# Performance work log

Measured on AMD Instinct MI355X. Metric: run time of the kernel, lower is better.

The kernel has to match this reference:

```python
import jax, jax.numpy as jnp
import numpy as np

B, V, T = 8, 16, 64
DIN, H, RH, K, TMP = 6, 256, 64, 2, 256
E = V * (V - 1)
NREL, NPOS = 7, 3  # 2D relative / positional feature counts

_edges = np.ones((V, V)) - np.eye(V)
SEND = jnp.asarray(np.where(_edges)[0])
RECV = jnp.asarray(np.where(_edges)[1])


def _w(k, shape, fan):
    return jax.random.normal(k, shape, jnp.float32) / np.sqrt(fan)


def setup_inputs() -> dict:
    key = jax.random.key(0)
    ks = jax.random.split(key, 20)
    d = {}
    d['rel_feat'] = jax.random.normal(ks[0], (B, V, T, DIN), jnp.float32)
    d['edge_attr_raw'] = jax.random.normal(ks[1], (B, E, T, NREL + DIN), jnp.float32)
    d['edge_pos'] = jax.random.normal(ks[2], (B, E, T, NPOS), jnp.float32)
    d['ef_w1'] = _w(ks[3], (H, NREL + DIN + NPOS), NREL + DIN + NPOS); d['ef_b1'] = jnp.full((H,), 0.1)
    d['ef_w2'] = _w(ks[4], (H, H), H); d['ef_b2'] = jnp.full((H,), 0.1)
    d['res_w'] = _w(ks[5], (H, DIN), DIN); d['res_b'] = jnp.full((H,), 0.1)
    d['m3_w1'] = _w(ks[6], (H, H), H); d['m3_b1'] = jnp.full((H,), 0.1)
    d['m3_w2'] = _w(ks[7], (H, H), H); d['m3_b2'] = jnp.full((H,), 0.1)
    d['m4_w1'] = _w(ks[8], (H, 3 * H), 3 * H); d['m4_b1'] = jnp.full((H,), 0.1)
    d['m4_w2'] = _w(ks[9], (H, H), H); d['m4_b2'] = jnp.full((H,), 0.1)
    d['f_wih'] = _w(ks[10], (4 * RH, H), H); d['f_whh'] = _w(ks[11], (4 * RH, RH), RH)
    d['f_bih'] = jnp.zeros((4 * RH,)); d['f_bhh'] = jnp.zeros((4 * RH,))
    d['r_wih'] = _w(ks[12], (4 * RH, H), H); d['r_whh'] = _w(ks[13], (4 * RH, RH), RH)
    d['r_bih'] = jnp.zeros((4 * RH,)); d['r_bhh'] = jnp.zeros((4 * RH,))
    d['p_w'] = _w(ks[14], (K, RH), RH); d['p_b'] = jnp.full((K,), 0.1)
    d['e_w1'] = _w(ks[15], (TMP, 2 * RH), 2 * RH); d['e_b1'] = jnp.full((TMP,), 0.1)
    d['e_w2'] = _w(ks[16], (K, TMP), TMP); d['e_b2'] = jnp.full((K,), 0.1)
    return d


def _lstm(x, wih, whh, bih, bhh):
    # x: [N, T, H] -> hidden sequence [N, T, RH]; torch gate order i, f, g, o
    n = x.shape[0]
    rh = whh.shape[1]
    xw = jnp.einsum('nth,gh->ntg', x, wih) + bih  # input GEMM hoisted out of scan

    def step(carry, xt):
        h, c = carry
        z = xt + h @ whh.T + bhh
        i, f, g, o = jnp.split(z, 4, axis=-1)
        c = jax.nn.sigmoid(f) * c + jax.nn.sigmoid(i) * jnp.tanh(g)
        h = jax.nn.sigmoid(o) * jnp.tanh(c)
        return (h, c), h

    h0 = jnp.zeros((n, rh), x.dtype)
    _, hs = jax.lax.scan(step, (h0, h0), jnp.swapaxes(xw, 0, 1))
    return jnp.swapaxes(hs, 0, 1)


def reference(rel_feat, edge_attr_raw, edge_pos, ef_w1, ef_b1, ef_w2, ef_b2, res_w, res_b, m3_w1, m3_b1, m3_w2, m3_b2, m4_w1, m4_b1, m4_w2, m4_b2, f_wih, f_whh, f_bih, f_bhh, r_wih, r_whh, r_bih, r_bhh, p_w, p_b, e_w1, e_b1, e_w2, e_b2):
    elu = jax.nn.elu
    # edge filter MLP: [B,E,T,NREL+DIN+NPOS] -> [B,E,T,H]
    ein = jnp.concatenate([edge_attr_raw, edge_pos], -1)
    edge_attr = elu(elu(ein @ ef_w1.T + ef_b1) @ ef_w2.T + ef_b2)
    # edge2node: scatter-sum over recv indices, normalized by (V-1)
    agg = jax.ops.segment_sum(jnp.moveaxis(edge_attr, 1, 0), RECV, num_segments=V)
    x = jnp.moveaxis(agg, 0, 1) / (V - 1) + (rel_feat @ res_w.T + res_b)
    # mlp3 on node embeddings
    x = elu(elu(x @ m3_w1.T + m3_b1) @ m3_w2.T + m3_b2)
    # node2edge gather + skip-concat with previous edge features -> mlp4
    x = jnp.concatenate([x[:, SEND], x[:, RECV], edge_attr], -1)  # [B,E,T,3H]
    x = elu(elu(x @ m4_w1.T + m4_b1) @ m4_w2.T + m4_b2)  # [B,E,T,H]
    # bidirectional LSTM over time, per edge
    seq = x.reshape(B * E, T, H)
    fwd = _lstm(seq, f_wih, f_whh, f_bih, f_bhh)
    rev = jnp.flip(_lstm(jnp.flip(seq, 1), r_wih, r_whh, r_bih, r_bhh), 1)
    prior = (fwd @ p_w.T + p_b).reshape(B, E, T, K).transpose(0, 2, 1, 3)  # [B,T,E,K]
    comb = jnp.concatenate([fwd, rev], -1)
    enc = (elu(comb @ e_w1.T + e_b1) @ e_w2.T + e_b2).reshape(B, E, T, K).transpose(0, 2, 1, 3)
    return prior, enc
```

## Files before the change

### kernel.cpp

```cpp
#include <hip/hip_runtime.h>
#include <cstdint>
#include <cstddef>
#include <type_traits>

#define B_ 8
#define V_ 16
#define T_ 64
#define E_ 240
#define H_ 256
#define RH_ 64
#define K_ 2
#define DIN_ 6
#define BET_ (B_*E_*T_)
#define BVT_ (B_*V_*T_)
#define BE_ (B_*E_)

typedef unsigned short ushort_t;
typedef unsigned int u32;
typedef __attribute__((ext_vector_type(8))) short bf16x8;
typedef __attribute__((ext_vector_type(4))) float f32x4;

__device__ __forceinline__ float eluf(float x) { return x > 0.f ? x : __expf(x) - 1.f; }
__device__ __forceinline__ float fsig(float x) { return 1.f / (1.f + __expf(-x)); }
__device__ __forceinline__ float ftanh_(float x) {
    float y = fminf(fmaxf(x, -8.f), 8.f);
    float e = __expf(2.f * y);
    return (e - 1.f) / (e + 1.f);
}
__device__ __forceinline__ float b2f(ushort_t u) {
    union { float f; uint32_t i; } v; v.i = ((uint32_t)u) << 16; return v.f;
}
__device__ __forceinline__ ushort_t f2b(float f) {
    union { float f; uint32_t i; } v; v.f = f;
    uint32_t r = (v.i + 0x7FFFu + ((v.i >> 16) & 1u)) >> 16;
    return (ushort_t)r;
}

__device__ __forceinline__ void gll16(const void* g, void* l) {
    __builtin_amdgcn_global_load_lds(
        (const __attribute__((address_space(1))) u32*)g,
        (__attribute__((address_space(3))) u32*)l, 16, 0, 0);
}

__global__ __launch_bounds__(512, 1) void gemm8_ef_k(
    const float* __restrict__ ear, const float* __restrict__ epos,
    const float* __restrict__ ef_w1, const float* __restrict__ ef_b1,
    const ushort_t* __restrict__ w_ef2, const float* __restrict__ ef_b2,
    ushort_t* __restrict__ EA)
{
    __shared__ ushort_t H1[8][8][512];
    __shared__ ushort_t slotB[4][16][512];
    const int tid = threadIdx.x;
    const int lane = tid & 63;
    const int w = tid >> 6;
    const int wm = w >> 2, wn = w & 3;
    const int m0 = blockIdx.x * 128;
    const int r16 = lane & 15, kq = lane >> 4;

    f32x4 acc[4][4];
    #pragma unroll
    for (int i = 0; i < 4; ++i)
        #pragma unroll
        for (int j = 0; j < 4; ++j)
            acc[i][j] = (f32x4){0.f, 0.f, 0.f, 0.f};
    {
        bf16x8 af[4], bfr[4];
        #pragma unroll
        for (int mf = 0; mf < 4; ++mf) {
            int m = m0 + wm * 64 + mf * 16 + r16;
            #pragma unroll
            for (int e = 0; e < 8; ++e) {
                float v = 0.f;
                if (kq < 2) {
                    int c = kq * 8 + e;
                    v = (c < 13) ? ear[(size_t)m * 13 + c] : epos[(size_t)m * 3 + (c - 13)];
                }
                af[mf][e] = (short)f2b(v);
            }
        }
        #pragma unroll
        for (int nf = 0; nf < 4; ++nf) {
            int n = wn * 64 + nf * 16 + r16;
            #pragma unroll
            for (int e = 0; e < 8; ++e) {
                float v = 0.f;
                if (kq < 2) v = ef_w1[(size_t)n * 16 + kq * 8 + e];
                bfr[nf][e] = (short)f2b(v);
            }
        }
        #pragma unroll
        for (int mf = 0; mf < 4; ++mf)
            #pragma unroll
            for (int nf = 0; nf < 4; ++nf)
                acc[mf][nf] = __builtin_amdgcn_mfma_f32_16x16x32_bf16(bfr[nf], af[mf], acc[mf][nf], 0, 0, 0);
    }

    const size_t bo0 = (size_t)(2 * w * 16 + r16) * 256 + kq * 8;
    const size_t bo1 = (size_t)((2 * w + 1) * 16 + r16) * 256 + kq * 8;
#define EF_ST(h) do { int sl_ = (h) & 3;                                    \
    gll16(w_ef2 + bo0 + (h) * 32, &slotB[sl_][2 * w][0]);                   \
    gll16(w_ef2 + bo1 + (h) * 32, &slotB[sl_][2 * w + 1][0]);               \
} while (0)

    EF_ST(0); EF_ST(1); EF_ST(2);

    #pragma unroll
    for (int mf = 0; mf < 4; ++mf) {
        #pragma unroll
        for (int nf = 0; nf < 4; ++nf) {
            int col = wn * 64 + nf * 16 + kq * 4;
            float4 bb = *(const float4*)&ef_b1[col];
            ushort4 o;
            o.x = f2b(eluf(acc[mf][nf][0] + bb.x));
            o.y = f2b(eluf(acc[mf][nf][1] + bb.y));
            o.z = f2b(eluf(acc[mf][nf][2] + bb.z));
            o.w = f2b(eluf(acc[mf][nf][3] + bb.w));
            int ktw = wn * 2 + (nf >> 1);
            int lanew = r16 + 16 * (((nf & 1) << 1) | (kq >> 1));
            *(ushort4*)&H1[wm * 4 + mf][ktw][lanew * 8 + (kq & 1) * 4] = o;
            acc[mf][nf] = (f32x4){0.f, 0.f, 0.f, 0.f};
        }
    }
    asm volatile("s_waitcnt lgkmcnt(0)" ::: "memory");
    asm volatile("s_waitcnt vmcnt(4)" ::: "memory");
    __builtin_amdgcn_s_barrier();

    #pragma unroll
    for (int h = 0; h < 8; ++h) {
        if (h + 3 < 8) EF_ST(h + 3);
        const int sl = h & 3;
        bf16x8 af[4], bfr[4];
        #pragma unroll
        for (int nf = 0; nf < 4; ++nf)
            bfr[nf] = *(const bf16x8*)&slotB[sl][wn * 4 + nf][lane * 8];
        #pragma unroll
        for (int mf = 0; mf < 4; ++mf)
            af[mf] = *(const bf16x8*)&H1[wm * 4 + mf][h][lane * 8];
        __builtin_amdgcn_s_setprio(1);
        #pragma unroll
        for (int mf = 0; mf < 4; ++mf)
            #pragma unroll
            for (int nf = 0; nf < 4; ++nf)
                acc[mf][nf] = __builtin_amdgcn_mfma_f32_16x16x32_bf16(bfr[nf], af[mf], acc[mf][nf], 0, 0, 0);
        __builtin_amdgcn_s_setprio(0);
        asm volatile("s_waitcnt lgkmcnt(0)" ::: "memory");
        if (h <= 4)      { asm volatile("s_waitcnt vmcnt(4)" ::: "memory"); }
        else if (h == 5) { asm volatile("s_waitcnt vmcnt(2)" ::: "memory"); }
        else if (h == 6) { asm volatile("s_waitcnt vmcnt(0)" ::: "memory"); }
        if (h < 7) __builtin_amdgcn_s_barrier();
    }
#undef EF_ST

    #pragma unroll
    for (int mf = 0; mf < 4; ++mf) {
        int row = m0 + wm * 64 + mf * 16 + r16;
        #pragma unroll
        for (int nf = 0; nf < 4; ++nf) {
            int col = wn * 64 + nf * 16 + kq * 4;
            float4 bb = *(const float4*)&ef_b2[col];
            ushort4 o;
            o.x = f2b(eluf(acc[mf][nf][0] + bb.x));
            o.y = f2b(eluf(acc[mf][nf][1] + bb.y));
            o.z = f2b(eluf(acc[mf][nf][2] + bb.z));
            o.w = f2b(eluf(acc[mf][nf][3] + bb.w));
            *(ushort4*)&EA[(size_t)row * 256 + col] = o;
        }
    }
}

__global__ __launch_bounds__(512, 1) void fused_gates9_k(
    ushort_t* __restrict__ T1, ushort_t* __restrict__ GR,
    const ushort_t* __restrict__ w_m42, const ushort_t* __restrict__ w_fih,
    const ushort_t* __restrict__ w_rih, const float* __restrict__ m4_b2,
    const float* __restrict__ f_bih, const float* __restrict__ f_bhh,
    const float* __restrict__ r_bih, const float* __restrict__ r_bhh)
{
    __shared__ ushort_t M2[8][8][512];
    __shared__ ushort_t slots[36864];
    const int tid = threadIdx.x;
    const int lane = tid & 63;
    const int w = tid >> 6;
    const int m0 = blockIdx.x * 128;
    const int r16 = lane & 15, kq = lane >> 4;

    const ushort_t* Ag = T1 + (size_t)(m0 + w * 16 + r16) * 256 + kq * 8;
    const size_t bo0 = (size_t)(2 * w * 16 + r16) * 256 + kq * 8;
    const size_t bo1 = (size_t)((2 * w + 1) * 16 + r16) * 256 + kq * 8;

    float4 bm4[2];
    #pragma unroll
    for (int nf = 0; nf < 2; ++nf)
        bm4[nf] = *(const float4*)&m4_b2[w * 32 + nf * 16 + kq * 4];
    const float* bi = (w < 4) ? f_bih : r_bih;
    const float* bh = (w < 4) ? f_bhh : r_bhh;
    float4 bg[4];
    #pragma unroll
    for (int nf = 0; nf < 4; ++nf) {
        int col = (w & 3) * 64 + nf * 16 + kq * 4;
        float4 a = *(const float4*)&bi[col];
        float4 b = *(const float4*)&bh[col];
        bg[nf] = (float4){a.x + b.x, a.y + b.y, a.z + b.z, a.w + b.w};
    }

    const ushort_t* WB = (w < 4) ? w_fih : w_rih;
    const int glb = (4 * w) & 15;

#define P0_ST(h) do { int sl_ = (h) % 3;                                    \
    gll16(Ag + (h) * 32, &slots[sl_ * 12288 + w * 512]);                    \
    gll16(w_m42 + bo0 + (h) * 32, &slots[sl_ * 12288 + 4096 + 2 * w * 512]);\
    gll16(w_m42 + bo1 + (h) * 32, &slots[sl_ * 12288 + 4096 + (2 * w + 1) * 512]); \
} while (0)
#define P1_ST(h) do { int sl_ = (h) & 1; int kk_ = (h) * 32;                \
    _Pragma("unroll")                                                       \
    for (int j = 0; j < 4; ++j)                                             \
        gll16(WB + (size_t)((glb + j) * 16 + r16) * 256 + kq * 8 + kk_,     \
              &slots[sl_ * 16384 + (4 * w + j) * 512]);                     \
} while (0)

    f32x4 acc0[8][2];
    #pragma unroll
    for (int i = 0; i < 8; ++i) { acc0[i][0] = (f32x4){0,0,0,0}; acc0[i][1] = (f32x4){0,0,0,0}; }

    P0_ST(0); P0_ST(1);
    asm volatile("s_waitcnt vmcnt(3)" ::: "memory");
    __builtin_amdgcn_s_barrier();

    for (int h = 0; h < 8; ++h) {
        if (h + 2 < 8) P0_ST(h + 2);
        const int sl = h % 3;
        bf16x8 af[8], bfr[2];
        #pragma unroll
        for (int mf = 0; mf < 8; ++mf)
            af[mf] = *(const bf16x8*)&slots[sl * 12288 + mf * 512 + lane * 8];
        #pragma unroll
        for (int nf = 0; nf < 2; ++nf)
            bfr[nf] = *(const bf16x8*)&slots[sl * 12288 + 4096 + (2 * w + nf) * 512 + lane * 8];
        __builtin_amdgcn_s_setprio(1);
        #pragma unroll
        for (int mf = 0; mf < 8; ++mf)
            #pragma unroll
            for (int nf = 0; nf < 2; ++nf)
                acc0[mf][nf] = __builtin_amdgcn_mfma_f32_16x16x32_bf16(bfr[nf], af[mf], acc0[mf][nf], 0, 0, 0);
        __builtin_amdgcn_s_setprio(0);
        asm volatile("s_waitcnt lgkmcnt(0)" ::: "memory");
        if (h <= 5)      { asm volatile("s_waitcnt vmcnt(3)" ::: "memory"); }
        else if (h == 6) { asm volatile("s_waitcnt vmcnt(0)" ::: "memory"); }
        if (h < 7) __builtin_amdgcn_s_barrier();
    }

    P1_ST(0);
    #pragma unroll
    for (int mf = 0; mf < 8; ++mf) {
        #pragma unroll
        for (int nf = 0; nf < 2; ++nf) {
            ushort4 o;
            o.x = f2b(eluf(acc0[mf][nf][0] + bm4[nf].x));
            o.y = f2b(eluf(acc0[mf][nf][1] + bm4[nf].y));
            o.z = f2b(eluf(acc0[mf][nf][2] + bm4[nf].z));
            o.w = f2b(eluf(acc0[mf][nf][3] + bm4[nf].w));
            int lanew = r16 + 16 * ((nf << 1) | (kq >> 1));
            *(ushort4*)&M2[mf][w][lanew * 8 + (kq & 1) * 4] = o;
        }
    }
    asm volatile("s_waitcnt lgkmcnt(0)" ::: "memory");
    asm volatile("s_waitcnt vmcnt(0)" ::: "memory");
    __builtin_amdgcn_s_barrier();

    f32x4 acc1[8][4];
    #pragma unroll
    for (int i = 0; i < 8; ++i)
        #pragma unroll
        for (int j = 0; j < 4; ++j)
            acc1[i][j] = (f32x4){0.f, 0.f, 0.f, 0.f};

    for (int h = 0; h < 8; ++h) {
        if (h + 1 < 8) P1_ST(h + 1);
        const int sl = h & 1;
        bf16x8 af[8], bfr[4];
        #pragma unroll
        for (int mf = 0; mf < 8; ++mf)
            af[mf] = *(const bf16x8*)&M2[mf][h][lane * 8];
        #pragma unroll
        for (int nf = 0; nf < 4; ++nf)
            bfr[nf] = *(const bf16x8*)&slots[sl * 16384 + (4 * w + nf) * 512 + lane * 8];
        __builtin_amdgcn_s_setprio(1);
        #pragma unroll
        for (int mf = 0; mf < 8; ++mf)
            #pragma unroll
            for (int nf = 0; nf < 4; ++nf)
                acc1[mf][nf] = __builtin_amdgcn_mfma_f32_16x16x32_bf16(bfr[nf], af[mf], acc1[mf][nf], 0, 0, 0);
        __builtin_amdgcn_s_setprio(0);
        asm volatile("s_waitcnt lgkmcnt(0)" ::: "memory");
        if (h + 1 < 8) { asm volatile("s_waitcnt vmcnt(0)" ::: "memory"); }
        if (h < 7) __builtin_amdgcn_s_barrier();
    }

    ushort_t* Wout = (w < 4) ? T1 : GR;
    #pragma unroll
    for (int mf = 0; mf < 8; ++mf) {
        int row = m0 + mf * 16 + r16;
        #pragma unroll
        for (int nf = 0; nf < 4; ++nf) {
            int col = (w & 3) * 64 + nf * 16 + kq * 4;
            ushort4 o;
            o.x = f2b(acc1[mf][nf][0] + bg[nf].x);
            o.y = f2b(acc1[mf][nf][1] + bg[nf].y);
            o.z = f2b(acc1[mf][nf][2] + bg[nf].z);
            o.w = f2b(acc1[mf][nf][3] + bg[nf].w);
            *(ushort4*)&Wout[(size_t)row * 256 + col] = o;
        }
    }
#undef P0_ST
#undef P1_ST
}

__global__ __launch_bounds__(512, 1) void gemm8_mlp3_k(
    const ushort_t* __restrict__ Xb, const ushort_t* __restrict__ w1,
    const float* __restrict__ b1, const ushort_t* __restrict__ w2,
    const float* __restrict__ b2, ushort_t* __restrict__ Out)
{
    __shared__ ushort_t H1[8][8][512];
    __shared__ ushort_t slots[36864];
    const int tid = threadIdx.x;
    const int lane = tid & 63;
    const int w = tid >> 6;
    const int m0 = blockIdx.x * 128;
    const int r16 = lane & 15, kq = lane >> 4;

    const ushort_t* Ag = Xb + (size_t)(m0 + w * 16 + r16) * 256 + kq * 8;
    const size_t bo0 = (size_t)(2 * w * 16 + r16) * 256 + kq * 8;
    const size_t bo1 = (size_t)((2 * w + 1) * 16 + r16) * 256 + kq * 8;

    float4 bb1[2], bb2[2];
    #pragma unroll
    for (int nf = 0; nf < 2; ++nf) {
        bb1[nf] = *(const float4*)&b1[w * 32 + nf * 16 + kq * 4];
        bb2[nf] = *(const float4*)&b2[w * 32 + nf * 16 + kq * 4];
    }

#define M3_ST0(h) do { int sl_ = (h) % 3;                                   \
    gll16(Ag + (h) * 32, &slots[sl_ * 12288 + w * 512]);                    \
    gll16(w1 + bo0 + (h) * 32, &slots[sl_ * 12288 + 4096 + 2 * w * 512]);   \
    gll16(w1 + bo1 + (h) * 32, &slots[sl_ * 12288 + 4096 + (2 * w + 1) * 512]); \
} while (0)
#define M3_ST1(h) do { int sl_ = (h) & 1; int kk_ = (h) * 32;               \
    gll16(w2 + bo0 + kk_, &slots[sl_ * 8192 + 2 * w * 512]);                \
    gll16(w2 + bo1 + kk_, &slots[sl_ * 8192 + (2 * w + 1) * 512]);          \
} while (0)

    f32x4 acc0[8][2];
    #pragma unroll
    for (int i = 0; i < 8; ++i) { acc0[i][0] = (f32x4){0,0,0,0}; acc0[i][1] = (f32x4){0,0,0,0}; }

    M3_ST0(0); M3_ST0(1);
    asm volatile("s_waitcnt vmcnt(3)" ::: "memory");
    __builtin_amdgcn_s_barrier();

    for (int h = 0; h < 8; ++h) {
        if (h + 2 < 8) M3_ST0(h + 2);
        const int sl = h % 3;
        bf16x8 af[8], bfr[2];
        #pragma unroll
        for (int mf = 0; mf < 8; ++mf)
            af[mf] = *(const bf16x8*)&slots[sl * 12288 + mf * 512 + lane * 8];
        #pragma unroll
        for (int nf = 0; nf < 2; ++nf)
            bfr[nf] = *(const bf16x8*)&slots[sl * 12288 + 4096 + (2 * w + nf) * 512 + lane * 8];
        #pragma unroll
        for (int mf = 0; mf < 8; ++mf)
            #pragma unroll
            for (int nf = 0; nf < 2; ++nf)
                acc0[mf][nf] = __builtin_amdgcn_mfma_f32_16x16x32_bf16(bfr[nf], af[mf], acc0[mf][nf], 0, 0, 0);
        asm volatile("s_waitcnt lgkmcnt(0)" ::: "memory");
        if (h <= 5)      { asm volatile("s_waitcnt vmcnt(3)" ::: "memory"); }
        else if (h == 6) { asm volatile("s_waitcnt vmcnt(0)" ::: "memory"); }
        if (h < 7) __builtin_amdgcn_s_barrier();
    }

    M3_ST1(0);
    #pragma unroll
    for (int mf = 0; mf < 8; ++mf) {
        #pragma unroll
        for (int nf = 0; nf < 2; ++nf) {
            ushort4 o;
            o.x = f2b(eluf(acc0[mf][nf][0] + bb1[nf].x));
            o.y = f2b(eluf(acc0[mf][nf][1] + bb1[nf].y));
            o.z = f2b(eluf(acc0[mf][nf][2] + bb1[nf].z));
            o.w = f2b(eluf(acc0[mf][nf][3] + bb1[nf].w));
            int lanew = r16 + 16 * ((nf << 1) | (kq >> 1));
            *(ushort4*)&H1[mf][w][lanew * 8 + (kq & 1) * 4] = o;
            acc0[mf][nf] = (f32x4){0.f, 0.f, 0.f, 0.f};
        }
    }
    asm volatile("s_waitcnt lgkmcnt(0)" ::: "memory");
    asm volatile("s_waitcnt vmcnt(0)" ::: "memory");
    __builtin_amdgcn_s_barrier();

    for (int h = 0; h < 8; ++h) {
        if (h + 1 < 8) M3_ST1(h + 1);
        const int sl = h & 1;
        bf16x8 af[8], bfr[2];
        #pragma unroll
        for (int mf = 0; mf < 8; ++mf)
            af[mf] = *(const bf16x8*)&H1[mf][h][lane * 8];
        #pragma unroll
        for (int nf = 0; nf < 2; ++nf)
            bfr[nf] = *(const bf16x8*)&slots[sl * 8192 + (2 * w + nf) * 512 + lane * 8];
        #pragma unroll
        for (int mf = 0; mf < 8; ++mf)
            #pragma unroll
            for (int nf = 0; nf < 2; ++nf)
                acc0[mf][nf] = __builtin_amdgcn_mfma_f32_16x16x32_bf16(bfr[nf], af[mf], acc0[mf][nf], 0, 0, 0);
        asm volatile("s_waitcnt lgkmcnt(0)" ::: "memory");
        if (h + 1 < 8) { asm volatile("s_waitcnt vmcnt(0)" ::: "memory"); }
        if (h < 7) __builtin_amdgcn_s_barrier();
    }

    #pragma unroll
    for (int mf = 0; mf < 8; ++mf) {
        int row = m0 + mf * 16 + r16;
        #pragma unroll
        for (int nf = 0; nf < 2; ++nf) {
            int col = w * 32 + nf * 16 + kq * 4;
            ushort4 o;
            o.x = f2b(eluf(acc0[mf][nf][0] + bb2[nf].x));
            o.y = f2b(eluf(acc0[mf][nf][1] + bb2[nf].y));
            o.z = f2b(eluf(acc0[mf][nf][2] + bb2[nf].z));
            o.w = f2b(eluf(acc0[mf][nf][3] + bb2[nf].w));
            *(ushort4*)&Out[(size_t)row * 256 + col] = o;
        }
    }
#undef M3_ST0
#undef M3_ST1
}

__global__ __launch_bounds__(512, 2) void gemm8_mlp4_k(
    const ushort_t* __restrict__ X2b, const ushort_t* __restrict__ EA,
    const ushort_t* __restrict__ Wt, const float* __restrict__ b1,
    ushort_t* __restrict__ C)
{
    __shared__ ushort_t lds[4][32][512];
    const int tid = threadIdx.x;
    const int lane = tid & 63;
    const int w = tid >> 6;
    const int wm = w >> 2, wn = w & 3;
    const int m0 = blockIdx.x * 256;
    const int r16 = lane & 15, kq = lane >> 4;
    constexpr int NH = 24;

    const ushort_t* AS[2]; const ushort_t* AR[2]; const ushort_t* AE[2];
    #pragma unroll
    for (int ff = 0; ff < 2; ++ff) {
        int f = w + ff * 8;
        int m = m0 + f * 16 + r16;
        int be = m >> 6, t = m & 63;
        int b = be / E_, e = be % E_;
        int s = e / (V_ - 1);
        int r0 = e % (V_ - 1);
        int rr = r0 + (r0 >= s ? 1 : 0);
        AS[ff] = X2b + ((size_t)((b * V_ + s) * T_ + t)) * H_ + kq * 8;
        AR[ff] = X2b + ((size_t)((b * V_ + rr) * T_ + t)) * H_ + kq * 8;
        AE[ff] = EA + (size_t)m * H_ + kq * 8;
    }
    const ushort_t* Bg0 = Wt + (size_t)(w * 16 + r16) * 768 + kq * 8;
    const ushort_t* Bg1 = Wt + (size_t)((w + 8) * 16 + r16) * 768 + kq * 8;

    f32x4 acc[8][4];
    #pragma unroll
    for (int i = 0; i < 8; ++i)
        #pragma unroll
        for (int j = 0; j < 4; ++j)
            acc[i][j] = (f32x4){0.f, 0.f, 0.f, 0.f};

#define STM(h) do { int sl_ = (h) & 3; int kk_ = (h) * 32;                  \
    int seg_ = kk_ >> 8, off_ = kk_ & 255;                                  \
    const ushort_t* a0_ = (seg_ == 0 ? AS[0] : seg_ == 1 ? AR[0] : AE[0]) + off_; \
    const ushort_t* a1_ = (seg_ == 0 ? AS[1] : seg_ == 1 ? AR[1] : AE[1]) + off_; \
    gll16(a0_, &lds[sl_][w][0]);                                            \
    gll16(a1_, &lds[sl_][w + 8][0]);                                        \
    gll16(Bg0 + kk_, &lds[sl_][16 + w][0]);                                 \
    gll16(Bg1 + kk_, &lds[sl_][16 + w + 8][0]);                             \
} while (0)

    STM(0); STM(1); STM(2);
    asm volatile("s_waitcnt vmcnt(8)" ::: "memory");
    __builtin_amdgcn_s_barrier();

    for (int h = 0; h < NH; ++h) {
        if (h + 3 < NH) STM(h + 3);
        const int sl = h & 3;
        bf16x8 bfr[4];
        #pragma unroll
        for (int nf = 0; nf < 4; ++nf)
            bfr[nf] = *(const bf16x8*)&lds[sl][16 + wn * 4 + nf][lane * 8];
        #pragma unroll
        for (int mh = 0; mh < 2; ++mh) {
            bf16x8 af[4];
            #pragma unroll
            for (int mf = 0; mf < 4; ++mf)
                af[mf] = *(const bf16x8*)&lds[sl][wm * 8 + mh * 4 + mf][lane * 8];
            __builtin_amdgcn_s_setprio(1);
            #pragma unroll
            for (int mf = 0; mf < 4; ++mf)
                #pragma unroll
                for (int nf = 0; nf < 4; ++nf)
                    acc[mh * 4 + mf][nf] = __builtin_amdgcn_mfma_f32_16x16x32_bf16(
                        bfr[nf], af[mf], acc[mh * 4 + mf][nf], 0, 0, 0);
            __builtin_amdgcn_s_setprio(0);
        }
        asm volatile("s_waitcnt lgkmcnt(0)" ::: "memory");
        if (h < NH - 3)       { asm volatile("s_waitcnt vmcnt(8)" ::: "memory"); }
        else if (h == NH - 3) { asm volatile("s_waitcnt vmcnt(4)" ::: "memory"); }
        else if (h == NH - 2) { asm volatile("s_waitcnt vmcnt(0)" ::: "memory"); }
        if (h < NH - 1) __builtin_amdgcn_s_barrier();
    }
#undef STM

    #pragma unroll
    for (int mi = 0; mi < 8; ++mi) {
        int mrow = m0 + wm * 128 + mi * 16 + r16;
        #pragma unroll
        for (int nf = 0; nf < 4; ++nf) {
            int nb = wn * 64 + nf * 16 + kq * 4;
            float4 bb = *(const float4*)&b1[nb];
            float v0 = eluf(acc[mi][nf][0] + bb.x);
            float v1 = eluf(acc[mi][nf][1] + bb.y);
            float v2 = eluf(acc[mi][nf][2] + bb.z);
            float v3 = eluf(acc[mi][nf][3] + bb.w);
            ushort4 o; o.x = f2b(v0); o.y = f2b(v1); o.z = f2b(v2); o.w = f2b(v3);
            *(ushort4*)&C[(size_t)mrow * 256 + nb] = o;
        }
    }
}

__global__ __launch_bounds__(256) void wconv_k(
    const float* __restrict__ ef_w2, const float* __restrict__ m4_w1,
    const float* __restrict__ m4_w2, const float* __restrict__ f_wih,
    const float* __restrict__ r_wih, const float* __restrict__ e_w1,
    const float* __restrict__ m3_w1, const float* __restrict__ m3_w2,
    ushort_t* __restrict__ Wb)
{
    int i = blockIdx.x * 256 + threadIdx.x;
    const float* src; int off;
    if (i < 65536)       { src = ef_w2; off = i; }
    else if (i < 262144) { src = m4_w1; off = i - 65536; }
    else if (i < 327680) { src = m4_w2; off = i - 262144; }
    else if (i < 393216) { src = f_wih; off = i - 327680; }
    else if (i < 458752) { src = r_wih; off = i - 393216; }
    else if (i < 491520) { src = e_w1;  off = i - 458752; }
    else if (i < 557056) { src = m3_w1; off = i - 491520; }
    else                 { src = m3_w2; off = i - 557056; }
    Wb[i] = f2b(src[off]);
}

__global__ __launch_bounds__(256) void e2n_k(
    const ushort_t* __restrict__ EA, const float* __restrict__ rel,
    const float* __restrict__ res_w, const float* __restrict__ res_b,
    ushort_t* __restrict__ X)
{
    const int idx = blockIdx.x;
    const int t = idx & (T_ - 1);
    const int bv = idx >> 6;
    const int v = bv & (V_ - 1);
    const int b = bv >> 4;
    const int h = threadIdx.x;
    float sum = 0.f;
    #pragma unroll
    for (int i = 0; i < V_; ++i) {
        if (i == v) continue;
        int jj = (v < i) ? v : v - 1;
        int e = i * (V_ - 1) + jj;
        sum += b2f(EA[(((size_t)(b * E_ + e)) * T_ + t) * H_ + h]);
    }
    const float* rp = rel + ((size_t)bv * T_ + t) * DIN_;
    float res = res_b[h];
    #pragma unroll
    for (int d = 0; d < DIN_; ++d) res += rp[d] * res_w[h * DIN_ + d];
    X[((size_t)bv * T_ + t) * H_ + h] = f2b(sum * (1.f / 15.f) + res);
}

__global__ __launch_bounds__(256) void lstm_mfma4_k(
    const ushort_t* __restrict__ Gf, const ushort_t* __restrict__ Gr,
    const float* __restrict__ whh_f, const float* __restrict__ whh_r,
    ushort_t* __restrict__ COMB)
{
    __shared__ ushort_t hlds[2][1024];
    const int dir = blockIdx.y;
    const ushort_t* G = dir ? Gr : Gf;
    const float* whh = dir ? whh_r : whh_f;
    const int tid = threadIdx.x;
    const int lane = tid & 63;
    const int w = tid >> 6;
    const int seq = lane & 15, kq = lane >> 4;
    const int be0 = blockIdx.x * 16;
    const int swz = (seq & 7) << 4;

    bf16x8 wf[4][2];
    #pragma unroll
    for (int a = 0; a < 4; ++a) {
        #pragma unroll
        for (int ks = 0; ks < 2; ++ks) {
            const float* p = whh + (size_t)((a * 4 + w) * 16 + seq) * 64 + ks * 32 + kq * 8;
            float4 x0 = *(const float4*)p;
            float4 x1 = *(const float4*)(p + 4);
            bf16x8 v;
            v[0] = (short)f2b(x0.x); v[1] = (short)f2b(x0.y);
            v[2] = (short)f2b(x0.z); v[3] = (short)f2b(x0.w);
            v[4] = (short)f2b(x1.x); v[5] = (short)f2b(x1.y);
            v[6] = (short)f2b(x1.z); v[7] = (short)f2b(x1.w);
            wf[a][ks] = v;
        }
    }

    const ushort_t* grow = G + ((size_t)(be0 + seq) * T_) * 256 + kq * 4;
    ushort_t* crow = COMB + ((size_t)(be0 + seq) * T_) * 128 + (dir ? 64 : 0) + 16 * w + 4 * kq;

    float c[4] = {};
    ushort4 gx[4];
    const int t0 = dir ? (T_ - 1) : 0;
    #pragma unroll
    for (int a = 0; a < 4; ++a)
        gx[a] = *(const ushort4*)(grow + (size_t)t0 * 256 + (a * 4 + w) * 16);

    for (int s = 0; s < T_; ++s) {
        const int t = dir ? (T_ - 1 - s) : s;
        f32x4 acc[4];
        #pragma unroll
        for (int a = 0; a < 4; ++a) {
            ushort4 g = gx[a];
            acc[a] = (f32x4){b2f(g.x), b2f(g.y), b2f(g.z), b2f(g.w)};
        }
        if (s < T_ - 1) {
            const int tn = dir ? (T_ - 2 - s) : (s + 1);
            #pragma unroll
            for (int a = 0; a < 4; ++a)
                gx[a] = *(const ushort4*)(grow + (size_t)tn * 256 + (a * 4 + w) * 16);
        }
        if (s) {
            bf16x8 af[2];
            #pragma unroll
            for (int ks = 0; ks < 2; ++ks) {
                int boff = (seq * 128 + ks * 64 + kq * 16) ^ swz;
                af[ks] = *(const bf16x8*)((const char*)hlds[(s - 1) & 1] + boff);
            }
            #pragma unroll
            for (int a = 0; a < 4; ++a) {
                acc[a] = __builtin_amdgcn_mfma_f32_16x16x32_bf16(wf[a][0], af[0], acc[a], 0, 0, 0);
                acc[a] = __builtin_amdgcn_mfma_f32_16x16x32_bf16(wf[a][1], af[1], acc[a], 0, 0, 0);
            }
        }
        float hh[4];
        #pragma unroll
        for (int r = 0; r < 4; ++r) {
            float zi = acc[0][r], zf = acc[1][r], zg = acc[2][r], zo = acc[3][r];
            float cc = fsig(zf) * c[r] + fsig(zi) * ftanh_(zg);
            c[r] = cc;
            hh[r] = fsig(zo) * ftanh_(cc);
        }
        ushort4 hv;
        hv.x = f2b(hh[0]); hv.y = f2b(hh[1]); hv.z = f2b(hh[2]); hv.w = f2b(hh[3]);
        int wb = (seq * 128 + 32 * w + 8 * kq) ^ swz;
        *(ushort4*)((char*)hlds[s & 1] + wb) = hv;
        *(ushort4*)(crow + (size_t)t * 128) = hv;
        asm volatile("s_waitcnt lgkmcnt(0)" ::: "memory");
        __builtin_amdgcn_sched_barrier(0);
        __builtin_amdgcn_s_barrier();
    }
}

__global__ __launch_bounds__(256) void prior_k(
    const ushort_t* __restrict__ COMB, const float* __restrict__ p_w,
    const float* __restrict__ p_b, float* __restrict__ out)
{
    const int row = blockIdx.x * 4 + (threadIdx.x >> 6);
    const int lane = threadIdx.x & 63;
    float hf = b2f(COMB[(size_t)row * 128 + lane]);
    float v0 = hf * p_w[lane];
    float v1 = hf * p_w[64 + lane];
    #pragma unroll
    for (int off = 32; off > 0; off >>= 1) {
        v0 += __shfl_down(v0, off, 64);
        v1 += __shfl_down(v1, off, 64);
    }
    if (lane == 0) {
        int t = row & (T_ - 1);
        int be = row >> 6;
        int e = be % E_, b = be / E_;
        size_t o = (((size_t)b * T_ + t) * E_ + e) * K_;
        out[o] = v0 + p_b[0];
        out[o + 1] = v1 + p_b[1];
    }
}

__global__ __launch_bounds__(512) void fused_enc_k(
    const ushort_t* __restrict__ COMB, const ushort_t* __restrict__ w_e1,
    const float* __restrict__ e_b1, const float* __restrict__ e_w2,
    const float* __restrict__ e_b2, float* __restrict__ out)
{
    __shared__ ushort_t sA[2][8][512];
    __shared__ ushort_t sW[2][16][512];
    __shared__ float part[128][4][2];
    const int tid = threadIdx.x;
    const int lane = tid & 63;
    const int w = tid >> 6;
    const int wr = w >> 2, wc = w & 3;
    const int m0 = blockIdx.x * 128;
    const int r16 = lane & 15, kq = lane >> 4;

    const ushort_t* Asrc = COMB + (size_t)(m0 + w * 16 + r16) * 128 + kq * 8;
    const size_t woffA = (size_t)((2 * w) * 16 + r16) * 128 + kq * 8;
    const size_t woffB = (size_t)((2 * w + 1) * 16 + r16) * 128 + kq * 8;

    float4 w2v[2][4];
    #pragma unroll
    for (int j = 0; j < 2; ++j)
        #pragma unroll
        for (int nf = 0; nf < 4; ++nf)
            w2v[j][nf] = *(const float4*)&e_w2[j * 256 + wc * 64 + nf * 16 + kq * 4];

    f32x4 acc[4][4];
    #pragma unroll
    for (int i = 0; i < 4; ++i)
        #pragma unroll
        for (int j = 0; j < 4; ++j)
            acc[i][j] = (f32x4){0.f, 0.f, 0.f, 0.f};

#define FE_STAGE(bufi, kt_) do {                                             \
    gll16(Asrc + (kt_) * 32, &sA[bufi][w][0]);                               \
    gll16(w_e1 + woffA + (kt_) * 32, &sW[bufi][2 * w][0]);                   \
    gll16(w_e1 + woffB + (kt_) * 32, &sW[bufi][2 * w + 1][0]);               \
} while (0)

    FE_STAGE(0, 0);
    asm volatile("s_waitcnt vmcnt(0)" ::: "memory");
    __builtin_amdgcn_s_barrier();

    for (int s = 0; s < 4; ++s) {
        const int buf = s & 1;
        if (s < 3) FE_STAGE(buf ^ 1, s + 1);
        bf16x8 af[4], bfr[4];
        #pragma unroll
        for (int mf = 0; mf < 4; ++mf)
            af[mf] = *(const bf16x8*)&sA[buf][wr * 4 + mf][lane * 8];
        #pragma unroll
        for (int nf = 0; nf < 4; ++nf)
            bfr[nf] = *(const bf16x8*)&sW[buf][wc * 4 + nf][lane * 8];
        #pragma unroll
        for (int mf = 0; mf < 4; ++mf)
            #pragma unroll
            for (int nf = 0; nf < 4; ++nf)
                acc[mf][nf] = __builtin_amdgcn_mfma_f32_16x16x32_bf16(bfr[nf], af[mf], acc[mf][nf], 0, 0, 0);
        asm volatile("s_waitcnt vmcnt(0)" ::: "memory");
        __builtin_amdgcn_s_barrier();
    }

    #pragma unroll
    for (int mf = 0; mf < 4; ++mf) {
        float s0 = 0.f, s1 = 0.f;
        #pragma unroll
        for (int nf = 0; nf < 4; ++nf) {
            int col = wc * 64 + nf * 16 + kq * 4;
            float4 bb = *(const float4*)&e_b1[col];
            float v0 = eluf(acc[mf][nf][0] + bb.x);
            float v1 = eluf(acc[mf][nf][1] + bb.y);
            float v2 = eluf(acc[mf][nf][2] + bb.z);
            float v3 = eluf(acc[mf][nf][3] + bb.w);
            s0 += v0 * w2v[0][nf].x + v1 * w2v[0][nf].y + v2 * w2v[0][nf].z + v3 * w2v[0][nf].w;
            s1 += v0 * w2v[1][nf].x + v1 * w2v[1][nf].y + v2 * w2v[1][nf].z + v3 * w2v[1][nf].w;
        }
        s0 += __shfl_xor(s0, 16, 64); s0 += __shfl_xor(s0, 32, 64);
        s1 += __shfl_xor(s1, 16, 64); s1 += __shfl_xor(s1, 32, 64);
        if (kq == 0) {
            part[wr * 64 + mf * 16 + r16][wc][0] = s0;
            part[wr * 64 + mf * 16 + r16][wc][1] = s1;
        }
    }
    __syncthreads();
    if (tid < 256) {
        int row = tid >> 1, k = tid & 1;
        float v = part[row][0][k] + part[row][1][k] + part[row][2][k] + part[row][3][k] + e_b2[k];
        int gr = m0 + row;
        int be = gr >> 6, t = gr & 63;
        int e = be % E_, b = be / E_;
        out[(size_t)(B_ * T_ * E_ * K_) + (((size_t)b * T_ + t) * E_ + e) * K_ + k] = v;
    }
#undef FE_STAGE
}

extern "C" void kernel_launch(void* const* d_in, const int* in_sizes, int n_in,
                              void* d_out, int out_size, void* d_ws, size_t ws_size,
                              hipStream_t stream)
{
    const float* rel    = (const float*)d_in[0];
    const float* ear    = (const float*)d_in[1];
    const float* epos   = (const float*)d_in[2];
    const float* ef_w1  = (const float*)d_in[3];
    const float* ef_b1  = (const float*)d_in[4];
    const float* ef_w2  = (const float*)d_in[5];
    const float* ef_b2  = (const float*)d_in[6];
    const float* res_w  = (const float*)d_in[7];
    const float* res_b  = (const float*)d_in[8];
    const float* m3_w1  = (const float*)d_in[9];
    const float* m3_b1  = (const float*)d_in[10];
    const float* m3_w2  = (const float*)d_in[11];
    const float* m3_b2  = (const float*)d_in[12];
    const float* m4_w1  = (const float*)d_in[13];
    const float* m4_b1  = (const float*)d_in[14];
    const float* m4_w2  = (const float*)d_in[15];
    const float* m4_b2  = (const float*)d_in[16];
    const float* f_wih  = (const float*)d_in[17];
    const float* f_whh  = (const float*)d_in[18];
    const float* f_bih  = (const float*)d_in[19];
    const float* f_bhh  = (const float*)d_in[20];
    const float* r_wih  = (const float*)d_in[21];
    const float* r_whh  = (const float*)d_in[22];
    const float* r_bih  = (const float*)d_in[23];
    const float* r_bhh  = (const float*)d_in[24];
    const float* p_w    = (const float*)d_in[25];
    const float* p_b    = (const float*)d_in[26];
    const float* e_w1   = (const float*)d_in[27];
    const float* e_b1   = (const float*)d_in[28];
    const float* e_w2   = (const float*)d_in[29];
    const float* e_b2   = (const float*)d_in[30];
    float* out = (float*)d_out;

    char* ws = (char*)d_ws;
    const size_t BIGB  = (size_t)BET_ * H_ * sizeof(ushort_t);
    const size_t COMBB = (size_t)BET_ * 128 * sizeof(ushort_t);
    const size_t X2BB  = (size_t)BVT_ * H_ * sizeof(ushort_t);
    ushort_t* R1   = (ushort_t*)(ws);
    ushort_t* R2   = (ushort_t*)(ws + BIGB);
    ushort_t* COMB = (ushort_t*)(ws + 2 * BIGB);
    ushort_t* X2b  = (ushort_t*)(ws + 2 * BIGB + COMBB);
    ushort_t* Wb   = (ushort_t*)(ws + 2 * BIGB + COMBB + X2BB);
    ushort_t* Xbf = (ushort_t*)(ws);
    const ushort_t* wb_ef2  = Wb + 0;
    const ushort_t* wb_m41  = Wb + 65536;
    const ushort_t* wb_m42  = Wb + 262144;
    const ushort_t* wb_fwih = Wb + 327680;
    const ushort_t* wb_rwih = Wb + 393216;
    const ushort_t* wb_ew1  = Wb + 458752;
    const ushort_t* wb_m31  = Wb + 491520;
    const ushort_t* wb_m32  = Wb + 557056;

    dim3 blk(256);
    dim3 blk8(512);
    dim3 g128(BET_ / 128);
    dim3 g256(BET_ / 256);

    wconv_k<<<2432, blk, 0, stream>>>(ef_w2, m4_w1, m4_w2, f_wih, r_wih, e_w1, m3_w1, m3_w2, Wb);
    gemm8_ef_k<<<g128, blk8, 0, stream>>>(ear, epos, ef_w1, ef_b1, wb_ef2, ef_b2, R2);
    e2n_k<<<BVT_, blk, 0, stream>>>(R2, rel, res_w, res_b, Xbf);
    gemm8_mlp3_k<<<BVT_ / 128, blk8, 0, stream>>>(Xbf, wb_m31, m3_b1, wb_m32, m3_b2, X2b);
    gemm8_mlp4_k<<<g256, blk8, 0, stream>>>(X2b, R2, wb_m41, m4_b1, R1);
    fused_gates9_k<<<g128, blk8, 0, stream>>>(
        R1, R2, wb_m42, wb_fwih, wb_rwih, m4_b2, f_bih, f_bhh, r_bih, r_bhh);
    lstm_mfma4_k<<<dim3(BE_ / 16, 2), blk, 0, stream>>>(R1, R2, f_whh, r_whh, COMB);
    prior_k<<<BET_ / 4, blk, 0, stream>>>(COMB, p_w, p_b, out);
    fused_enc_k<<<g128, blk8, 0, stream>>>(COMB, wb_ew1, e_b1, e_w2, e_b2, out);
}
```

Before: 448.6 us.

## Split fused m4/gate-input kernel into three generic tiled GEMM launches

Replaces the fused kernel with three launches of a new templated 256x256-tile bf16 MFMA GEMM. That kernel uses a 4-stage global_load_lds pipeline and launch bounds allowing two blocks per CU. The three launches are the mlp4 second layer, the forward LSTM input projection and the reverse projection, which writes R2 in place. The intent is better MFMA utilization and occupancy than the two-phase fused kernel, which ran with one block per CU. The cost is that the mlp4 output now makes a round trip through global memory, and the input is re-read by two separate launches.

```diff
diff --git a/kernel.cpp b/kernel.cpp
--- a/kernel.cpp
+++ b/kernel.cpp
@@ -40,6 +40,96 @@
     __builtin_amdgcn_global_load_lds(
         (const __attribute__((address_space(1))) u32*)g,
         (__attribute__((address_space(3))) u32*)l, 16, 0, 0);
+}
+
+template<int KD, int ACT>
+__global__ __launch_bounds__(512, 2) void gemm8_k(
+    const ushort_t* __restrict__ A, const ushort_t* __restrict__ Wt,
+    const float* __restrict__ b1, const float* __restrict__ b2,
+    ushort_t* __restrict__ C)
+{
+    __shared__ ushort_t lds[4][32][512];
+    const int tid = threadIdx.x;
+    const int lane = tid & 63;
+    const int w = tid >> 6;
+    const int wm = w >> 2, wn = w & 3;
+    const int m0 = blockIdx.x * 256;
+    const int r16 = lane & 15, kq = lane >> 4;
+    constexpr int NH = KD / 32;
+
+    const ushort_t* Ag0 = A + (size_t)(m0 + w * 16 + r16) * KD + kq * 8;
+    const ushort_t* Ag1 = A + (size_t)(m0 + (w + 8) * 16 + r16) * KD + kq * 8;
+    const ushort_t* Bg0 = Wt + (size_t)(w * 16 + r16) * KD + kq * 8;
+    const ushort_t* Bg1 = Wt + (size_t)((w + 8) * 16 + r16) * KD + kq * 8;
+
+    f32x4 acc[8][4];
+    #pragma unroll
+    for (int i = 0; i < 8; ++i)
+        #pragma unroll
+        for (int j = 0; j < 4; ++j)
+            acc[i][j] = (f32x4){0.f, 0.f, 0.f, 0.f};
+
+#define ST8(h) do { int sl_ = (h) & 3; int kk_ = (h) * 32;                  \
+    gll16(Ag0 + kk_, &lds[sl_][w][0]);                                      \
+    gll16(Ag1 + kk_, &lds[sl_][w + 8][0]);                                  \
+    gll16(Bg0 + kk_, &lds[sl_][16 + w][0]);                                 \
+    gll16(Bg1 + kk_, &lds[sl_][16 + w + 8][0]);                             \
+} while (0)
+
+    ST8(0); ST8(1); ST8(2);
+    asm volatile("s_waitcnt vmcnt(8)" ::: "memory");
+    __builtin_amdgcn_s_barrier();
+
+    for (int h = 0; h < NH; ++h) {
+        if (h + 3 < NH) ST8(h + 3);
+        const int sl = h & 3;
+        bf16x8 bfr[4];
+        #pragma unroll
+        for (int nf = 0; nf < 4; ++nf)
+            bfr[nf] = *(const bf16x8*)&lds[sl][16 + wn * 4 + nf][lane * 8];
+        #pragma unroll
+        for (int mh = 0; mh < 2; ++mh) {
+            bf16x8 af[4];
+            #pragma unroll
+            for (int mf = 0; mf < 4; ++mf)
+                af[mf] = *(const bf16x8*)&lds[sl][wm * 8 + mh * 4 + mf][lane * 8];
+            __builtin_amdgcn_s_setprio(1);
+            #pragma unroll
+            for (int mf = 0; mf < 4; ++mf)
+                #pragma unroll
+                for (int nf = 0; nf < 4; ++nf)
+                    acc[mh * 4 + mf][nf] = __builtin_amdgcn_mfma_f32_16x16x32_bf16(
+                        bfr[nf], af[mf], acc[mh * 4 + mf][nf], 0, 0, 0);
+            __builtin_amdgcn_s_setprio(0);
+        }
+        asm volatile("s_waitcnt lgkmcnt(0)" ::: "memory");
+        if (h < NH - 3)       { asm volatile("s_waitcnt vmcnt(8)" ::: "memory"); }
+        else if (h == NH - 3) { asm volatile("s_waitcnt vmcnt(4)" ::: "memory"); }
+        else if (h == NH - 2) { asm volatile("s_waitcnt vmcnt(0)" ::: "memory"); }
+        if (h < NH - 1) __builtin_amdgcn_s_barrier();
+    }
+#undef ST8
+
+    #pragma unroll
+    for (int mi = 0; mi < 8; ++mi) {
+        int mrow = m0 + wm * 128 + mi * 16 + r16;
+        #pragma unroll
+        for (int nf = 0; nf < 4; ++nf) {
+            int nb = wn * 64 + nf * 16 + kq * 4;
+            float4 bb = *(const float4*)&b1[nb];
+            if (b2) {
+                float4 b2v = *(const float4*)&b2[nb];
+                bb.x += b2v.x; bb.y += b2v.y; bb.z += b2v.z; bb.w += b2v.w;
+            }
+            float v0 = acc[mi][nf][0] + bb.x;
+            float v1 = acc[mi][nf][1] + bb.y;
+            float v2 = acc[mi][nf][2] + bb.z;
+            float v3 = acc[mi][nf][3] + bb.w;
+            if (ACT) { v0 = eluf(v0); v1 = eluf(v1); v2 = eluf(v2); v3 = eluf(v3); }
+            ushort4 o; o.x = f2b(v0); o.y = f2b(v1); o.z = f2b(v2); o.w = f2b(v3);
+            *(ushort4*)&C[(size_t)mrow * 256 + nb] = o;
+        }
+    }
 }
 
 __global__ __launch_bounds__(512, 1) void gemm8_ef_k(
@@ -166,152 +256,6 @@
             *(ushort4*)&EA[(size_t)row * 256 + col] = o;
         }
     }
-}
-
-__global__ __launch_bounds__(512, 1) void fused_gates9_k(
-    ushort_t* __restrict__ T1, ushort_t* __restrict__ GR,
-    const ushort_t* __restrict__ w_m42, const ushort_t* __restrict__ w_fih,
-    const ushort_t* __restrict__ w_rih, const float* __restrict__ m4_b2,
-    const float* __restrict__ f_bih, const float* __restrict__ f_bhh,
-    const float* __restrict__ r_bih, const float* __restrict__ r_bhh)
-{
-    __shared__ ushort_t M2[8][8][512];
-    __shared__ ushort_t slots[36864];
-    const int tid = threadIdx.x;
-    const int lane = tid & 63;
-    const int w = tid >> 6;
-    const int m0 = blockIdx.x * 128;
-    const int r16 = lane & 15, kq = lane >> 4;
-
-    const ushort_t* Ag = T1 + (size_t)(m0 + w * 16 + r16) * 256 + kq * 8;
-    const size_t bo0 = (size_t)(2 * w * 16 + r16) * 256 + kq * 8;
-    const size_t bo1 = (size_t)((2 * w + 1) * 16 + r16) * 256 + kq * 8;
-
-    float4 bm4[2];
-    #pragma unroll
-    for (int nf = 0; nf < 2; ++nf)
-        bm4[nf] = *(const float4*)&m4_b2[w * 32 + nf * 16 + kq * 4];
-    const float* bi = (w < 4) ? f_bih : r_bih;
-    const float* bh = (w < 4) ? f_bhh : r_bhh;
-    float4 bg[4];
-    #pragma unroll
-    for (int nf = 0; nf < 4; ++nf) {
-        int col = (w & 3) * 64 + nf * 16 + kq * 4;
-        float4 a = *(const float4*)&bi[col];
-        float4 b = *(const float4*)&bh[col];
-        bg[nf] = (float4){a.x + b.x, a.y + b.y, a.z + b.z, a.w + b.w};
-    }
-
-    const ushort_t* WB = (w < 4) ? w_fih : w_rih;
-    const int glb = (4 * w) & 15;
-
-#define P0_ST(h) do { int sl_ = (h) % 3;                                    \
-    gll16(Ag + (h) * 32, &slots[sl_ * 12288 + w * 512]);                    \
-    gll16(w_m42 + bo0 + (h) * 32, &slots[sl_ * 12288 + 4096 + 2 * w * 512]);\
-    gll16(w_m42 + bo1 + (h) * 32, &slots[sl_ * 12288 + 4096 + (2 * w + 1) * 512]); \
-} while (0)
-#define P1_ST(h) do { int sl_ = (h) & 1; int kk_ = (h) * 32;                \
-    _Pragma("unroll")                                                       \
-    for (int j = 0; j < 4; ++j)                                             \
-        gll16(WB + (size_t)((glb + j) * 16 + r16) * 256 + kq * 8 + kk_,     \
-              &slots[sl_ * 16384 + (4 * w + j) * 512]);                     \
-} while (0)
-
-    f32x4 acc0[8][2];
-    #pragma unroll
-    for (int i = 0; i < 8; ++i) { acc0[i][0] = (f32x4){0,0,0,0}; acc0[i][1] = (f32x4){0,0,0,0}; }
-
-    P0_ST(0); P0_ST(1);
-    asm volatile("s_waitcnt vmcnt(3)" ::: "memory");
-    __builtin_amdgcn_s_barrier();
-
-    for (int h = 0; h < 8; ++h) {
-        if (h + 2 < 8) P0_ST(h + 2);
-        const int sl = h % 3;
-        bf16x8 af[8], bfr[2];
-        #pragma unroll
-        for (int mf = 0; mf < 8; ++mf)
-            af[mf] = *(const bf16x8*)&slots[sl * 12288 + mf * 512 + lane * 8];
-        #pragma unroll
-        for (int nf = 0; nf < 2; ++nf)
-            bfr[nf] = *(const bf16x8*)&slots[sl * 12288 + 4096 + (2 * w + nf) * 512 + lane * 8];
-        __builtin_amdgcn_s_setprio(1);
-        #pragma unroll
-        for (int mf = 0; mf < 8; ++mf)
-            #pragma unroll
-            for (int nf = 0; nf < 2; ++nf)
-                acc0[mf][nf] = __builtin_amdgcn_mfma_f32_16x16x32_bf16(bfr[nf], af[mf], acc0[mf][nf], 0, 0, 0);
-        __builtin_amdgcn_s_setprio(0);
-        asm volatile("s_waitcnt lgkmcnt(0)" ::: "memory");
-        if (h <= 5)      { asm volatile("s_waitcnt vmcnt(3)" ::: "memory"); }
-        else if (h == 6) { asm volatile("s_waitcnt vmcnt(0)" ::: "memory"); }
-        if (h < 7) __builtin_amdgcn_s_barrier();
-    }
-
-    P1_ST(0);
-    #pragma unroll
-    for (int mf = 0; mf < 8; ++mf) {
-        #pragma unroll
-        for (int nf = 0; nf < 2; ++nf) {
-            ushort4 o;
-            o.x = f2b(eluf(acc0[mf][nf][0] + bm4[nf].x));
-            o.y = f2b(eluf(acc0[mf][nf][1] + bm4[nf].y));
-            o.z = f2b(eluf(acc0[mf][nf][2] + bm4[nf].z));
-            o.w = f2b(eluf(acc0[mf][nf][3] + bm4[nf].w));
-            int lanew = r16 + 16 * ((nf << 1) | (kq >> 1));
-            *(ushort4*)&M2[mf][w][lanew * 8 + (kq & 1) * 4] = o;
-        }
-    }
-    asm volatile("s_waitcnt lgkmcnt(0)" ::: "memory");
-    asm volatile("s_waitcnt vmcnt(0)" ::: "memory");
-    __builtin_amdgcn_s_barrier();
-
-    f32x4 acc1[8][4];
-    #pragma unroll
-    for (int i = 0; i < 8; ++i)
-        #pragma unroll
-        for (int j = 0; j < 4; ++j)
-            acc1[i][j] = (f32x4){0.f, 0.f, 0.f, 0.f};
-
-    for (int h = 0; h < 8; ++h) {
-        if (h + 1 < 8) P1_ST(h + 1);
-        const int sl = h & 1;
-        bf16x8 af[8], bfr[4];
-        #pragma unroll
-        for (int mf = 0; mf < 8; ++mf)
-            af[mf] = *(const bf16x8*)&M2[mf][h][lane * 8];
-        #pragma unroll
-        for (int nf = 0; nf < 4; ++nf)
-            bfr[nf] = *(const bf16x8*)&slots[sl * 16384 + (4 * w + nf) * 512 + lane * 8];
-        __builtin_amdgcn_s_setprio(1);
-        #pragma unroll
-        for (int mf = 0; mf < 8; ++mf)
-            #pragma unroll
-            for (int nf = 0; nf < 4; ++nf)
-                acc1[mf][nf] = __builtin_amdgcn_mfma_f32_16x16x32_bf16(bfr[nf], af[mf], acc1[mf][nf], 0, 0, 0);
-        __builtin_amdgcn_s_setprio(0);
-        asm volatile("s_waitcnt lgkmcnt(0)" ::: "memory");
-        if (h + 1 < 8) { asm volatile("s_waitcnt vmcnt(0)" ::: "memory"); }
-        if (h < 7) __builtin_amdgcn_s_barrier();
-    }
-
-    ushort_t* Wout = (w < 4) ? T1 : GR;
-    #pragma unroll
-    for (int mf = 0; mf < 8; ++mf) {
-        int row = m0 + mf * 16 + r16;
-        #pragma unroll
-        for (int nf = 0; nf < 4; ++nf) {
-            int col = (w & 3) * 64 + nf * 16 + kq * 4;
-            ushort4 o;
-            o.x = f2b(acc1[mf][nf][0] + bg[nf].x);
-            o.y = f2b(acc1[mf][nf][1] + bg[nf].y);
-            o.z = f2b(acc1[mf][nf][2] + bg[nf].z);
-            o.w = f2b(acc1[mf][nf][3] + bg[nf].w);
-            *(ushort4*)&Wout[(size_t)row * 256 + col] = o;
-        }
-    }
-#undef P0_ST
-#undef P1_ST
 }
 
 __global__ __launch_bounds__(512, 1) void gemm8_mlp3_k(
@@ -853,8 +797,9 @@
     e2n_k<<<BVT_, blk, 0, stream>>>(R2, rel, res_w, res_b, Xbf);
     gemm8_mlp3_k<<<BVT_ / 128, blk8, 0, stream>>>(Xbf, wb_m31, m3_b1, wb_m32, m3_b2, X2b);
     gemm8_mlp4_k<<<g256, blk8, 0, stream>>>(X2b, R2, wb_m41, m4_b1, R1);
-    fused_gates9_k<<<g128, blk8, 0, stream>>>(
-        R1, R2, wb_m42, wb_fwih, wb_rwih, m4_b2, f_bih, f_bhh, r_bih, r_bhh);
+    gemm8_k<256, 1><<<g256, blk8, 0, stream>>>(R1, wb_m42, m4_b2, nullptr, R2);
+    gemm8_k<256, 0><<<g256, blk8, 0, stream>>>(R2, wb_fwih, f_bih, f_bhh, R1);
+    gemm8_k<256, 0><<<g256, blk8, 0, stream>>>(R2, wb_rwih, r_bih, r_bhh, R2);
     lstm_mfma4_k<<<dim3(BE_ / 16, 2), blk, 0, stream>>>(R1, R2, f_whh, r_whh, COMB);
     prior_k<<<BET_ / 4, blk, 0, stream>>>(COMB, p_w, p_b, out);
     fused_enc_k<<<g128, blk8, 0, stream>>>(COMB, wb_ew1, e_b1, e_w2, e_b2, out);
```

Result: faster. 424.0 us (-5.5%).
